# Kernel tuning notes

Measured on AMD Instinct MI355X. Metric: run time of the kernel, lower is better.

The kernel has to match this reference:

```python
import jax, jax.numpy as jnp
import numpy as np

B, N, D, H, W, OUT = 2, 2048, 128, 8, 4, 256

def setup_inputs() -> dict:
    key = jax.random.key(0)
    ks = jax.random.split(key, 8)
    s = 0.02
    return {
        "nodefeatures": jax.random.normal(ks[0], (B, N, D), jnp.float32),
        "nodeadj": jax.random.uniform(ks[1], (B, N, N, W), jnp.float32),
        "Wq": jax.random.normal(ks[2], (H, D, D), jnp.float32) * s,
        "bq": jnp.zeros((H, D), jnp.float32),
        "Wk": jax.random.normal(ks[3], (H, D, D), jnp.float32) * s,
        "bk": jnp.zeros((H, D), jnp.float32),
        "Wv": jax.random.normal(ks[4], (H, D, D), jnp.float32) * s,
        "bv": jnp.zeros((H, D), jnp.float32),
        "Wout": jax.random.normal(ks[5], (H * D, OUT), jnp.float32) * s,
        "bout": jnp.zeros((OUT,), jnp.float32),
    }

def reference(nodefeatures, nodeadj, Wq, bq, Wk, bk, Wv, bv, Wout, bout):
    # Per-head linear projections, all heads at once: [B,H,N,D]
    q = jnp.einsum('bnd,hde->bhne', nodefeatures, Wq) + bq[None, :, None, :]
    k = jnp.einsum('bnd,hde->bhne', nodefeatures, Wk) + bk[None, :, None, :]
    v = jnp.einsum('bnd,hde->bhne', nodefeatures, Wv) + bv[None, :, None, :]
    # Original scales by k.shape[1]**0.5 == sqrt(N) (node count, not head dim)
    scores = jnp.einsum('bhnd,bhmd->bhnm', q, k) / jnp.sqrt(jnp.asarray(N, q.dtype))
    # (scores[...,None] * nodeadj).sum(-1) == scores * nodeadj.sum(-1)
    scores = scores * nodeadj.sum(-1)[:, None, :, :]  # [B,H,N,N]
    attn = jax.nn.softmax(scores, axis=-1)  # torch softmax(dim=2) on [B,N,N] == key axis
    o = jnp.einsum('bhnm,bhmd->bhnd', attn, v)
    o = jnp.moveaxis(o, 1, 2).reshape(B, N, H * D)  # concat heads along feature dim
    return o @ Wout + bout
```

## Files before the change

### kernel.cpp

```cpp
#include <hip/hip_runtime.h>
#include <hip/hip_bf16.h>

#define BB 2
#define NN 2048
#define DD 128
#define HH 8
#define OUTD 256
#define SCALE 0.022097086912079612f

typedef __bf16 bf16x8 __attribute__((ext_vector_type(8)));
typedef float f32x4 __attribute__((ext_vector_type(4)));
typedef _Float16 f16x8 __attribute__((ext_vector_type(8)));

__device__ __forceinline__ unsigned short f2bf(float f) {
    union { float f; unsigned int u; } v; v.f = f;
    unsigned int r = (v.u + 0x7FFFu + ((v.u >> 16) & 1u)) >> 16;
    return (unsigned short)r;
}
__device__ __forceinline__ float bf2f(unsigned short s) {
    union { unsigned int u; float f; } v; v.u = ((unsigned int)s) << 16;
    return v.f;
}
__device__ __forceinline__ void gl_lds16(const unsigned short* g, unsigned short* l) {
    __builtin_amdgcn_global_load_lds(
        (const __attribute__((address_space(1))) unsigned int*)g,
        (__attribute__((address_space(3))) unsigned int*)l,
        16, 0, 0);
}

__global__ void prep_kernel(const float* __restrict__ X,
                            const float* __restrict__ Wq,
                            const float* __restrict__ Wk,
                            const float* __restrict__ Wv,
                            const float* __restrict__ Wout,
                            unsigned short* __restrict__ Xb,
                            unsigned short* __restrict__ WT,
                            unsigned short* __restrict__ WoutT)
{
    const int NX  = BB * NN * DD;
    const int NW  = 3 * HH * DD * DD;
    const int NWO = (HH * DD) * OUTD;
    int idx = blockIdx.x * blockDim.x + threadIdx.x;
    if (idx < NX) {
        Xb[idx] = f2bf(X[idx]);
    } else if (idx < NX + NW) {
        int i = idx - NX;
        int mat = i / (HH * DD * DD);
        int r   = i % (HH * DD * DD);
        int h = r / (DD * DD);
        int j = r % (DD * DD);
        int e = j / DD;
        int d = j % DD;
        const float* Wm = (mat == 0) ? Wq : ((mat == 1) ? Wk : Wv);
        WT[i] = f2bf(Wm[h * DD * DD + d * DD + e]);
    } else if (idx < NX + NW + NWO) {
        int i = idx - NX - NW;
        int o = i / (HH * DD);
        int k = i % (HH * DD);
        WoutT[i] = f2bf(Wout[k * OUTD + o]);
    }
}

__global__ void adjsum_kernel(const float4* __restrict__ adj, unsigned short* __restrict__ s) {
    int idx = blockIdx.x * blockDim.x + threadIdx.x;
    float4 a = adj[idx];
    s[idx] = f2bf((a.x + a.y) + (a.z + a.w));
}

__global__ __launch_bounds__(256) void proj_kernel(
    const unsigned short* __restrict__ Xb,
    const unsigned short* __restrict__ WT,
    const float* __restrict__ bq, const float* __restrict__ bk, const float* __restrict__ bv,
    unsigned short* __restrict__ Qo, unsigned short* __restrict__ Ko,
    unsigned short* __restrict__ Vt)
{
    const int mat = blockIdx.z;
    const int bh  = blockIdx.y;
    const int b = bh >> 3, h = bh & 7;
    const int n0 = blockIdx.x * 64;
    const int tid = threadIdx.x;
    const int lane = tid & 63, wv = tid >> 6;
    const int m = lane & 15, quad = lane >> 4;

    __shared__ unsigned short Wlds[128 * 136];

    const unsigned short* Wg = WT + ((size_t)mat * HH + h) * (DD * DD);
    #pragma unroll
    for (int i = tid; i < 128 * 16; i += 256) {
        int r = i >> 4, c = i & 15;
        *(uint4*)&Wlds[r * 136 + c * 8] = *(const uint4*)(Wg + r * 128 + c * 8);
    }

    const int row = n0 + wv * 16 + m;
    const unsigned short* Xr = Xb + ((size_t)b * NN + row) * DD;
    bf16x8 af[4];
    #pragma unroll
    for (int kc = 0; kc < 4; ++kc)
        af[kc] = *(const bf16x8*)(Xr + kc * 32 + quad * 8);

    __syncthreads();

    f32x4 acc[8];
    #pragma unroll
    for (int et = 0; et < 8; ++et) acc[et] = (f32x4){0.f, 0.f, 0.f, 0.f};

    #pragma unroll
    for (int kc = 0; kc < 4; ++kc) {
        #pragma unroll
        for (int et = 0; et < 8; ++et) {
            bf16x8 bfrg = *(const bf16x8*)&Wlds[(et * 16 + m) * 136 + kc * 32 + quad * 8];
            acc[et] = __builtin_amdgcn_mfma_f32_16x16x32_bf16(af[kc], bfrg, acc[et], 0, 0, 0);
        }
    }

    const float* bias = (mat == 0) ? bq : ((mat == 1) ? bk : bv);
    if (mat != 2) {
        #pragma unroll
        for (int et = 0; et < 8; ++et) {
            int e = et * 16 + m;
            float bb = bias[h * DD + e];
            #pragma unroll
            for (int reg = 0; reg < 4; ++reg) {
                int r = n0 + wv * 16 + quad * 4 + reg;
                unsigned short v16 = f2bf(acc[et][reg] + bb);
                if (mat == 0) Qo[((size_t)bh * NN + r) * DD + e] = v16;
                else          Ko[((size_t)bh * NN + r) * DD + e] = v16;
            }
        }
    } else {
        __syncthreads();
        #pragma unroll
        for (int et = 0; et < 8; ++et) {
            int e = et * 16 + m;
            float bb = bias[h * DD + e];
            #pragma unroll
            for (int reg = 0; reg < 4; ++reg)
                Wlds[(wv * 16 + quad * 4 + reg) * 136 + e] = f2bf(acc[et][reg] + bb);
        }
        __syncthreads();
        const int e = tid >> 1, nh = tid & 1;
        #pragma unroll
        for (int j = 0; j < 4; ++j) {
            unsigned short tmp[8];
            #pragma unroll
            for (int kk = 0; kk < 8; ++kk)
                tmp[kk] = Wlds[(nh * 32 + j * 8 + kk) * 136 + e];
            *(uint4*)(Vt + ((size_t)bh * DD + e) * NN + n0 + nh * 32 + j * 8) = *(uint4*)tmp;
        }
    }
}

__global__ __launch_bounds__(256, 2) void attn_kernel(
    const unsigned short* __restrict__ Q,
    const unsigned short* __restrict__ K,
    const unsigned short* __restrict__ Vt,
    const unsigned short* __restrict__ adjs,
    _Float16* __restrict__ Opart,
    float* __restrict__ Lpart)
{
    const int x = blockIdx.x;
    const int h = blockIdx.y;
    const int ks = x & 1, qt = (x >> 1) & 15, b = x >> 5;
    const int bh = b * HH + h;
    const int q0 = qt * 128;
    const int kstart = ks * 1024;
    const int tid = threadIdx.x;
    const int lane = tid & 63, wv = tid >> 6;
    const int m = lane & 15, quad = lane >> 4;

    __shared__ unsigned short Kb[2][32 * 128];
    __shared__ unsigned short Vb[2][128 * 32];
    __shared__ unsigned short Plds[4][16 * 40];

    const unsigned short* Kbase = K + (size_t)bh * NN * DD;
    const unsigned short* Vbase = Vt + (size_t)bh * DD * NN;

    bf16x8 qf[2][4];
    #pragma unroll
    for (int qg = 0; qg < 2; ++qg) {
        const unsigned short* Qr = Q + ((size_t)bh * NN + q0 + wv * 32 + qg * 16 + m) * DD;
        #pragma unroll
        for (int kc = 0; kc < 4; ++kc)
            qf[qg][kc] = *(const bf16x8*)(Qr + kc * 32 + quad * 8);
    }

    f32x4 o[2][8];
    #pragma unroll
    for (int qg = 0; qg < 2; ++qg)
        #pragma unroll
        for (int dt = 0; dt < 8; ++dt) o[qg][dt] = (f32x4){0.f, 0.f, 0.f, 0.f};
    float li[2][4] = {{0.f,0.f,0.f,0.f},{0.f,0.f,0.f,0.f}};

    const unsigned short* Abase = adjs + ((size_t)b * NN + q0 + wv * 32 + quad * 4) * NN;

    const int kr4 = lane >> 4, kc16 = lane & 15;
    const int vr16 = lane >> 2, vc4 = lane & 3;

    #define STAGE(buf, kbase_)                                                              \
        {                                                                                   \
            _Pragma("unroll")                                                               \
            for (int j2 = 0; j2 < 2; ++j2) {                                                \
                const int j = wv * 2 + j2;                                                  \
                const int krow = j * 4 + kr4;                                               \
                gl_lds16(Kbase + (size_t)((kbase_) + krow) * DD + ((kc16 ^ (krow & 15)) * 8),\
                         &Kb[buf][j * 512]);                                                \
                const int vrow = j * 16 + vr16;                                             \
                gl_lds16(Vbase + (size_t)vrow * NN + (kbase_) + ((vc4 ^ ((vr16 >> 1) & 3)) * 8),\
                         &Vb[buf][j * 512]);                                                \
            }                                                                               \
        }

    STAGE(0, kstart);
    __syncthreads();

    for (int kt = 0; kt < 32; ++kt) {
        const int cb = kt & 1, nb = cb ^ 1;
        const int k0 = kstart + kt * 32;

        float areg[2][2][4];
        #pragma unroll
        for (int qg = 0; qg < 2; ++qg)
            #pragma unroll
            for (int nt = 0; nt < 2; ++nt)
                #pragma unroll
                for (int reg = 0; reg < 4; ++reg)
                    areg[qg][nt][reg] =
                        bf2f(Abase[(size_t)(qg * 16 + reg) * NN + k0 + nt * 16 + m]) * SCALE;

        if (kt + 1 < 32) STAGE(nb, k0 + 32);

        #pragma unroll
        for (int qg = 0; qg < 2; ++qg) {
            f32x4 s[2];
            s[0] = (f32x4){0.f, 0.f, 0.f, 0.f};
            s[1] = (f32x4){0.f, 0.f, 0.f, 0.f};
            #pragma unroll
            for (int kc = 0; kc < 4; ++kc) {
                #pragma unroll
                for (int nt = 0; nt < 2; ++nt) {
                    bf16x8 kf = *(const bf16x8*)&Kb[cb][(nt * 16 + m) * 128 + (((kc * 4 + quad) ^ m) * 8)];
                    s[nt] = __builtin_amdgcn_mfma_f32_16x16x32_bf16(qf[qg][kc], kf, s[nt], 0, 0, 0);
                }
            }

            #pragma unroll
            for (int nt = 0; nt < 2; ++nt) {
                #pragma unroll
                for (int reg = 0; reg < 4; ++reg) {
                    float p = __expf(s[nt][reg] * areg[qg][nt][reg]);
                    li[qg][reg] += p;
                    Plds[wv][(quad * 4 + reg) * 40 + nt * 16 + m] = f2bf(p);
                }
            }

            bf16x8 pf = *(const bf16x8*)&Plds[wv][m * 40 + quad * 8];
            #pragma unroll
            for (int dt = 0; dt < 8; ++dt) {
                bf16x8 vf = *(const bf16x8*)&Vb[cb][(dt * 16 + m) * 32 + ((quad ^ ((m >> 1) & 3)) * 8)];
                o[qg][dt] = __builtin_amdgcn_mfma_f32_16x16x32_bf16(pf, vf, o[qg][dt], 0, 0, 0);
            }
        }

        __syncthreads();
    }
    #undef STAGE

    #pragma unroll
    for (int qg = 0; qg < 2; ++qg) {
        #pragma unroll
        for (int reg = 0; reg < 4; ++reg) {
            float t = li[qg][reg];
            t += __shfl_xor(t, 1);
            t += __shfl_xor(t, 2);
            t += __shfl_xor(t, 4);
            t += __shfl_xor(t, 8);
            li[qg][reg] = t;
        }
        const int rbase = q0 + wv * 32 + qg * 16 + quad * 4;
        if (m == 0) {
            #pragma unroll
            for (int reg = 0; reg < 4; ++reg)
                Lpart[((size_t)ks * (BB * HH) + bh) * NN + rbase + reg] = li[qg][reg];
        }
        #pragma unroll
        for (int reg = 0; reg < 4; ++reg) {
            const size_t obase = (((size_t)ks * (BB * HH) + bh) * NN + rbase + reg) * DD;
            #pragma unroll
            for (int dt = 0; dt < 8; ++dt)
                Opart[obase + dt * 16 + m] = (_Float16)o[qg][dt][reg];
        }
    }
}

__global__ __launch_bounds__(256) void out_kernel(
    const _Float16* __restrict__ Op,
    const float* __restrict__ Lp,
    const unsigned short* __restrict__ WoutT,
    const float* __restrict__ bout,
    float* __restrict__ out)
{
    const int m0 = blockIdx.x * 64;
    const int c0 = blockIdx.y * 64;
    const int tid = threadIdx.x;
    const int lane = tid & 63, wv = tid >> 6;
    const int m = lane & 15, quad = lane >> 4;

    __shared__ unsigned short Wlds[64 * 136];

    f32x4 acc[4];
    #pragma unroll
    for (int nt = 0; nt < 4; ++nt) acc[nt] = (f32x4){0.f, 0.f, 0.f, 0.f};

    const int r = m0 + wv * 16 + m;
    const int b = r >> 11, n = r & (NN - 1);

    for (int kc = 0; kc < 8; ++kc) {
        #pragma unroll
        for (int i = tid; i < 64 * 16; i += 256) {
            int rr = i >> 4, c = i & 15;
            *(uint4*)&Wlds[rr * 136 + c * 8] =
                *(const uint4*)(WoutT + (size_t)(c0 + rr) * (HH * DD) + kc * 128 + c * 8);
        }
        const int bh = b * HH + kc;
        const float linv = 1.0f / (Lp[(size_t)bh * NN + n] +
                                   Lp[(size_t)(BB * HH + bh) * NN + n]);
        const size_t obase0 = ((size_t)bh * NN + n) * DD;
        const size_t obase1 = ((size_t)(BB * HH + bh) * NN + n) * DD;
        __syncthreads();
        #pragma unroll
        for (int j = 0; j < 4; ++j) {
            f16x8 a0 = *(const f16x8*)(Op + obase0 + j * 32 + quad * 8);
            f16x8 a1 = *(const f16x8*)(Op + obase1 + j * 32 + quad * 8);
            unsigned short pa[8];
            #pragma unroll
            for (int i = 0; i < 8; ++i)
                pa[i] = f2bf(((float)a0[i] + (float)a1[i]) * linv);
            bf16x8 afr = *(const bf16x8*)pa;
            #pragma unroll
            for (int nt = 0; nt < 4; ++nt) {
                bf16x8 bfr = *(const bf16x8*)&Wlds[(nt * 16 + m) * 136 + j * 32 + quad * 8];
                acc[nt] = __builtin_amdgcn_mfma_f32_16x16x32_bf16(afr, bfr, acc[nt], 0, 0, 0);
            }
        }
        __syncthreads();
    }

    #pragma unroll
    for (int nt = 0; nt < 4; ++nt) {
        int oc = c0 + nt * 16 + m;
        float bb = bout[oc];
        #pragma unroll
        for (int reg = 0; reg < 4; ++reg) {
            int rr = m0 + wv * 16 + quad * 4 + reg;
            out[(size_t)rr * OUTD + oc] = acc[nt][reg] + bb;
        }
    }
}

extern "C" void kernel_launch(void* const* d_in, const int* in_sizes, int n_in,
                              void* d_out, int out_size, void* d_ws, size_t ws_size,
                              hipStream_t stream)
{
    const float* X    = (const float*)d_in[0];
    const float* adj  = (const float*)d_in[1];
    const float* Wq   = (const float*)d_in[2];
    const float* bq   = (const float*)d_in[3];
    const float* Wk   = (const float*)d_in[4];
    const float* bk   = (const float*)d_in[5];
    const float* Wv   = (const float*)d_in[6];
    const float* bv   = (const float*)d_in[7];
    const float* Wout = (const float*)d_in[8];
    const float* bout = (const float*)d_in[9];
    float* out = (float*)d_out;

    char* ws = (char*)d_ws;
    unsigned short* Xb    = (unsigned short*)(ws);
    unsigned short* WT    = (unsigned short*)(ws + 1048576);
    unsigned short* WoutT = (unsigned short*)(ws + 1835008);
    unsigned short* Q     = (unsigned short*)(ws + 2359296);
    unsigned short* Kp    = (unsigned short*)(ws + 10747904);
    unsigned short* Vt    = (unsigned short*)(ws + 19136512);
    unsigned short* AsumB = (unsigned short*)(ws + 27525120);
    _Float16*       Opart = (_Float16*)(ws + 44302336);
    float*          Lpart = (float*)(ws);

    prep_kernel<<<4608, 256, 0, stream>>>(X, Wq, Wk, Wv, Wout, Xb, WT, WoutT);
    adjsum_kernel<<<(BB * NN * NN) / 256, 256, 0, stream>>>((const float4*)adj, AsumB);
    proj_kernel<<<dim3(NN / 64, BB * HH, 3), 256, 0, stream>>>(Xb, WT, bq, bk, bv, Q, Kp, Vt);
    attn_kernel<<<dim3(64, HH), 256, 0, stream>>>(Q, Kp, Vt, AsumB, Opart, Lpart);
    out_kernel<<<dim3((BB * NN) / 64, OUTD / 64), 256, 0, stream>>>(Opart, Lpart, WoutT, bout, out);
}
```

Baseline: 314.3 us.

## Vectorize weight prep, remap attention blocks per XCD, split combine from output GEMM

```diff
diff --git a/kernel.cpp b/kernel.cpp
--- a/kernel.cpp
+++ b/kernel.cpp
@@ -10,7 +10,7 @@
 
 typedef __bf16 bf16x8 __attribute__((ext_vector_type(8)));
 typedef float f32x4 __attribute__((ext_vector_type(4)));
-typedef _Float16 f16x8 __attribute__((ext_vector_type(8)));
+typedef _Float16 f16x4 __attribute__((ext_vector_type(4)));
 
 __device__ __forceinline__ unsigned short f2bf(float f) {
     union { float f; unsigned int u; } v; v.f = f;
@@ -28,36 +28,69 @@
         16, 0, 0);
 }
 
-__global__ void prep_kernel(const float* __restrict__ X,
-                            const float* __restrict__ Wq,
-                            const float* __restrict__ Wk,
-                            const float* __restrict__ Wv,
-                            const float* __restrict__ Wout,
-                            unsigned short* __restrict__ Xb,
-                            unsigned short* __restrict__ WT,
-                            unsigned short* __restrict__ WoutT)
-{
-    const int NX  = BB * NN * DD;
-    const int NW  = 3 * HH * DD * DD;
-    const int NWO = (HH * DD) * OUTD;
-    int idx = blockIdx.x * blockDim.x + threadIdx.x;
-    if (idx < NX) {
-        Xb[idx] = f2bf(X[idx]);
-    } else if (idx < NX + NW) {
-        int i = idx - NX;
-        int mat = i / (HH * DD * DD);
-        int r   = i % (HH * DD * DD);
-        int h = r / (DD * DD);
-        int j = r % (DD * DD);
-        int e = j / DD;
-        int d = j % DD;
+__global__ __launch_bounds__(256) void prep_kernel(
+    const float* __restrict__ X,
+    const float* __restrict__ Wq,
+    const float* __restrict__ Wk,
+    const float* __restrict__ Wv,
+    const float* __restrict__ Wout,
+    unsigned short* __restrict__ Xb,
+    unsigned short* __restrict__ WT,
+    unsigned short* __restrict__ WoutT)
+{
+    __shared__ unsigned short T[128 * 136];
+    const int bid = blockIdx.x;
+    const int t = threadIdx.x;
+
+    if (bid < 512) {
+        int i4 = (bid * 256 + t) * 4;
+        float4 v = *(const float4*)(X + i4);
+        unsigned short u[4] = {f2bf(v.x), f2bf(v.y), f2bf(v.z), f2bf(v.w)};
+        *(ushort4*)(Xb + i4) = *(const ushort4*)u;
+    } else if (bid < 536) {
+        const int mh = bid - 512;
+        const int mat = mh >> 3, h = mh & 7;
         const float* Wm = (mat == 0) ? Wq : ((mat == 1) ? Wk : Wv);
-        WT[i] = f2bf(Wm[h * DD * DD + d * DD + e]);
-    } else if (idx < NX + NW + NWO) {
-        int i = idx - NX - NW;
-        int o = i / (HH * DD);
-        int k = i % (HH * DD);
-        WoutT[i] = f2bf(Wout[k * OUTD + o]);
+        Wm += (size_t)h * DD * DD;
+        #pragma unroll
+        for (int i = 0; i < 16; ++i) {
+            int lin = i * 256 + t;
+            int d = lin >> 5, e = (lin & 31) * 4;
+            float4 v = *(const float4*)(Wm + (size_t)d * DD + e);
+            unsigned short u[4] = {f2bf(v.x), f2bf(v.y), f2bf(v.z), f2bf(v.w)};
+            *(uint2*)&T[d * 136 + e] = *(const uint2*)u;
+        }
+        __syncthreads();
+        const int e = t >> 1, nh = t & 1;
+        unsigned short* Wo = WT + ((size_t)mat * HH + h) * (DD * DD) + (size_t)e * DD + nh * 64;
+        #pragma unroll
+        for (int j = 0; j < 8; ++j) {
+            unsigned short tmp[8];
+            #pragma unroll
+            for (int k = 0; k < 8; ++k)
+                tmp[k] = T[(nh * 64 + j * 8 + k) * 136 + e];
+            *(uint4*)(Wo + j * 8) = *(const uint4*)tmp;
+        }
+    } else {
+        const int kb = bid - 536;
+        #pragma unroll
+        for (int i = 0; i < 16; ++i) {
+            int lin = i * 256 + t;
+            int k = lin >> 6, o = (lin & 63) * 4;
+            float4 v = *(const float4*)(Wout + (size_t)(kb * 64 + k) * OUTD + o);
+            unsigned short u[4] = {f2bf(v.x), f2bf(v.y), f2bf(v.z), f2bf(v.w)};
+            *(uint2*)&T[k * 264 + o] = *(const uint2*)u;
+        }
+        __syncthreads();
+        unsigned short* Wo = WoutT + (size_t)t * (HH * DD) + kb * 64;
+        #pragma unroll
+        for (int j = 0; j < 8; ++j) {
+            unsigned short tmp[8];
+            #pragma unroll
+            for (int k = 0; k < 8; ++k)
+                tmp[k] = T[(j * 8 + k) * 264 + t];
+            *(uint4*)(Wo + j * 8) = *(const uint4*)tmp;
+        }
     }
 }
 
@@ -158,9 +191,12 @@
     _Float16* __restrict__ Opart,
     float* __restrict__ Lpart)
 {
-    const int x = blockIdx.x;
-    const int h = blockIdx.y;
-    const int ks = x & 1, qt = (x >> 1) & 15, b = x >> 5;
+    const int L = blockIdx.x;
+    const int xcd = L & 7, W = L >> 3;
+    const int b  = (xcd >> 2) & 1;
+    const int ks = (xcd >> 1) & 1;
+    const int h  = (xcd & 1) * 4 + (W & 3);
+    const int qt = W >> 2;
     const int bh = b * HH + h;
     const int q0 = qt * 128;
     const int kstart = ks * 1024;
@@ -170,7 +206,7 @@
 
     __shared__ unsigned short Kb[2][32 * 128];
     __shared__ unsigned short Vb[2][128 * 32];
-    __shared__ unsigned short Plds[4][16 * 40];
+    __shared__ unsigned short Plds[4][2][16 * 40];
 
     const unsigned short* Kbase = K + (size_t)bh * NN * DD;
     const unsigned short* Vbase = Vt + (size_t)bh * DD * NN;
@@ -229,36 +265,37 @@
 
         if (kt + 1 < 32) STAGE(nb, k0 + 32);
 
-        #pragma unroll
-        for (int qg = 0; qg < 2; ++qg) {
-            f32x4 s[2];
-            s[0] = (f32x4){0.f, 0.f, 0.f, 0.f};
-            s[1] = (f32x4){0.f, 0.f, 0.f, 0.f};
-            #pragma unroll
-            for (int kc = 0; kc < 4; ++kc) {
-                #pragma unroll
-                for (int nt = 0; nt < 2; ++nt) {
-                    bf16x8 kf = *(const bf16x8*)&Kb[cb][(nt * 16 + m) * 128 + (((kc * 4 + quad) ^ m) * 8)];
-                    s[nt] = __builtin_amdgcn_mfma_f32_16x16x32_bf16(qf[qg][kc], kf, s[nt], 0, 0, 0);
-                }
+        f32x4 s[2][2];
+        s[0][0] = (f32x4){0.f,0.f,0.f,0.f}; s[0][1] = (f32x4){0.f,0.f,0.f,0.f};
+        s[1][0] = (f32x4){0.f,0.f,0.f,0.f}; s[1][1] = (f32x4){0.f,0.f,0.f,0.f};
+        #pragma unroll
+        for (int kc = 0; kc < 4; ++kc) {
+            #pragma unroll
+            for (int nt = 0; nt < 2; ++nt) {
+                bf16x8 kf = *(const bf16x8*)&Kb[cb][(nt * 16 + m) * 128 + (((kc * 4 + quad) ^ m) * 8)];
+                s[0][nt] = __builtin_amdgcn_mfma_f32_16x16x32_bf16(qf[0][kc], kf, s[0][nt], 0, 0, 0);
+                s[1][nt] = __builtin_amdgcn_mfma_f32_16x16x32_bf16(qf[1][kc], kf, s[1][nt], 0, 0, 0);
             }
-
-            #pragma unroll
-            for (int nt = 0; nt < 2; ++nt) {
+        }
+
+        #pragma unroll
+        for (int qg = 0; qg < 2; ++qg)
+            #pragma unroll
+            for (int nt = 0; nt < 2; ++nt)
                 #pragma unroll
                 for (int reg = 0; reg < 4; ++reg) {
-                    float p = __expf(s[nt][reg] * areg[qg][nt][reg]);
+                    float p = __expf(s[qg][nt][reg] * areg[qg][nt][reg]);
                     li[qg][reg] += p;
-                    Plds[wv][(quad * 4 + reg) * 40 + nt * 16 + m] = f2bf(p);
+                    Plds[wv][qg][(quad * 4 + reg) * 40 + nt * 16 + m] = f2bf(p);
                 }
-            }
-
-            bf16x8 pf = *(const bf16x8*)&Plds[wv][m * 40 + quad * 8];
-            #pragma unroll
-            for (int dt = 0; dt < 8; ++dt) {
-                bf16x8 vf = *(const bf16x8*)&Vb[cb][(dt * 16 + m) * 32 + ((quad ^ ((m >> 1) & 3)) * 8)];
-                o[qg][dt] = __builtin_amdgcn_mfma_f32_16x16x32_bf16(pf, vf, o[qg][dt], 0, 0, 0);
-            }
+
+        bf16x8 pf0 = *(const bf16x8*)&Plds[wv][0][m * 40 + quad * 8];
+        bf16x8 pf1 = *(const bf16x8*)&Plds[wv][1][m * 40 + quad * 8];
+        #pragma unroll
+        for (int dt = 0; dt < 8; ++dt) {
+            bf16x8 vf = *(const bf16x8*)&Vb[cb][(dt * 16 + m) * 32 + ((quad ^ ((m >> 1) & 3)) * 8)];
+            o[0][dt] = __builtin_amdgcn_mfma_f32_16x16x32_bf16(pf0, vf, o[0][dt], 0, 0, 0);
+            o[1][dt] = __builtin_amdgcn_mfma_f32_16x16x32_bf16(pf1, vf, o[1][dt], 0, 0, 0);
         }
 
         __syncthreads();
@@ -292,27 +329,47 @@
     }
 }
 
+__global__ void combine_kernel(const _Float16* __restrict__ Op,
+                               const float* __restrict__ Lp,
+                               unsigned short* __restrict__ Ocat)
+{
+    const int SPLIT_OFF = BB * HH * NN * DD;
+    int t = blockIdx.x * blockDim.x + threadIdx.x;
+    int e0 = t * 4;
+    int row = e0 >> 7;
+    float l = 1.0f / (Lp[row] + Lp[row + BB * HH * NN]);
+    f16x4 a = *(const f16x4*)(Op + e0);
+    f16x4 c = *(const f16x4*)(Op + SPLIT_OFF + e0);
+    int bh = row >> 11, n = row & (NN - 1);
+    int b = bh >> 3, h = bh & 7;
+    size_t obase = ((size_t)(b * NN + n)) * (HH * DD) + h * DD + (e0 & (DD - 1));
+    unsigned short u[4];
+    #pragma unroll
+    for (int i = 0; i < 4; ++i)
+        u[i] = f2bf(((float)a[i] + (float)c[i]) * l);
+    *(ushort4*)(Ocat + obase) = *(ushort4*)u;
+}
+
 __global__ __launch_bounds__(256) void out_kernel(
-    const _Float16* __restrict__ Op,
-    const float* __restrict__ Lp,
+    const unsigned short* __restrict__ Ocat,
     const unsigned short* __restrict__ WoutT,
     const float* __restrict__ bout,
     float* __restrict__ out)
 {
-    const int m0 = blockIdx.x * 64;
+    const int m0 = blockIdx.x * 32;
     const int c0 = blockIdx.y * 64;
     const int tid = threadIdx.x;
     const int lane = tid & 63, wv = tid >> 6;
     const int m = lane & 15, quad = lane >> 4;
+    const int mg = wv & 1, cg = wv >> 1;
 
     __shared__ unsigned short Wlds[64 * 136];
 
-    f32x4 acc[4];
-    #pragma unroll
-    for (int nt = 0; nt < 4; ++nt) acc[nt] = (f32x4){0.f, 0.f, 0.f, 0.f};
-
-    const int r = m0 + wv * 16 + m;
-    const int b = r >> 11, n = r & (NN - 1);
+    f32x4 acc[2];
+    acc[0] = (f32x4){0.f,0.f,0.f,0.f};
+    acc[1] = (f32x4){0.f,0.f,0.f,0.f};
+
+    const unsigned short* Orow = Ocat + (size_t)(m0 + mg * 16 + m) * (HH * DD);
 
     for (int kc = 0; kc < 8; ++kc) {
         #pragma unroll
@@ -321,24 +378,13 @@
             *(uint4*)&Wlds[rr * 136 + c * 8] =
                 *(const uint4*)(WoutT + (size_t)(c0 + rr) * (HH * DD) + kc * 128 + c * 8);
         }
-        const int bh = b * HH + kc;
-        const float linv = 1.0f / (Lp[(size_t)bh * NN + n] +
-                                   Lp[(size_t)(BB * HH + bh) * NN + n]);
-        const size_t obase0 = ((size_t)bh * NN + n) * DD;
-        const size_t obase1 = ((size_t)(BB * HH + bh) * NN + n) * DD;
         __syncthreads();
         #pragma unroll
         for (int j = 0; j < 4; ++j) {
-            f16x8 a0 = *(const f16x8*)(Op + obase0 + j * 32 + quad * 8);
-            f16x8 a1 = *(const f16x8*)(Op + obase1 + j * 32 + quad * 8);
-            unsigned short pa[8];
-            #pragma unroll
-            for (int i = 0; i < 8; ++i)
-                pa[i] = f2bf(((float)a0[i] + (float)a1[i]) * linv);
-            bf16x8 afr = *(const bf16x8*)pa;
-            #pragma unroll
-            for (int nt = 0; nt < 4; ++nt) {
-                bf16x8 bfr = *(const bf16x8*)&Wlds[(nt * 16 + m) * 136 + j * 32 + quad * 8];
+            bf16x8 afr = *(const bf16x8*)(Orow + kc * 128 + j * 32 + quad * 8);
+            #pragma unroll
+            for (int nt = 0; nt < 2; ++nt) {
+                bf16x8 bfr = *(const bf16x8*)&Wlds[(cg * 32 + nt * 16 + m) * 136 + j * 32 + quad * 8];
                 acc[nt] = __builtin_amdgcn_mfma_f32_16x16x32_bf16(afr, bfr, acc[nt], 0, 0, 0);
             }
         }
@@ -346,12 +392,12 @@
     }
 
     #pragma unroll
-    for (int nt = 0; nt < 4; ++nt) {
-        int oc = c0 + nt * 16 + m;
+    for (int nt = 0; nt < 2; ++nt) {
+        int oc = c0 + cg * 32 + nt * 16 + m;
         float bb = bout[oc];
         #pragma unroll
         for (int reg = 0; reg < 4; ++reg) {
-            int rr = m0 + wv * 16 + quad * 4 + reg;
+            int rr = m0 + mg * 16 + quad * 4 + reg;
             out[(size_t)rr * OUTD + oc] = acc[nt][reg] + bb;
         }
     }
@@ -382,11 +428,13 @@
     unsigned short* Vt    = (unsigned short*)(ws + 19136512);
     unsigned short* AsumB = (unsigned short*)(ws + 27525120);
     _Float16*       Opart = (_Float16*)(ws + 44302336);
+    unsigned short* Ocat  = (unsigned short*)(ws + 61079552);
     float*          Lpart = (float*)(ws);
 
-    prep_kernel<<<4608, 256, 0, stream>>>(X, Wq, Wk, Wv, Wout, Xb, WT, WoutT);
+    prep_kernel<<<552, 256, 0, stream>>>(X, Wq, Wk, Wv, Wout, Xb, WT, WoutT);
     adjsum_kernel<<<(BB * NN * NN) / 256, 256, 0, stream>>>((const float4*)adj, AsumB);
     proj_kernel<<<dim3(NN / 64, BB * HH, 3), 256, 0, stream>>>(Xb, WT, bq, bk, bv, Q, Kp, Vt);
-    attn_kernel<<<dim3(64, HH), 256, 0, stream>>>(Q, Kp, Vt, AsumB, Opart, Lpart);
-    out_kernel<<<dim3((BB * NN) / 64, OUTD / 64), 256, 0, stream>>>(Opart, Lpart, WoutT, bout, out);
-}
+    attn_kernel<<<512, 256, 0, stream>>>(Q, Kp, Vt, AsumB, Opart, Lpart);
+    combine_kernel<<<(BB * HH * NN * DD / 4) / 256, 256, 0, stream>>>(Opart, Lpart, Ocat);
+    out_kernel<<<dim3((BB * NN) / 32, OUTD / 64), 256, 0, stream>>>(Ocat, WoutT, bout, out);
+}
```

Result: no change. 312.6 us (-0.5%).
